# Kernel tuning notes

Measured on AMD Instinct MI355X. Metric: run time of the kernel, lower is better.

## Reference

```python
import jax, jax.numpy as jnp
import numpy as np

B, S, D = 4, 2048, 1024
E, H, K = 32, 128, 2


def setup_inputs() -> dict:
    key = jax.random.key(0)
    k1, k2, k3, k4 = jax.random.split(key, 4)
    scale_d = 1.0 / np.sqrt(D)
    scale_h = 1.0 / np.sqrt(H)
    return {
        "x": jax.random.normal(k1, (B, S, D), dtype=jnp.float32),
        "w_sel": jax.random.normal(k2, (E, D), dtype=jnp.float32) * scale_d,      # router Linear weight [E, D]
        "w_keys": jax.random.normal(k3, (E, D, H), dtype=jnp.float32) * scale_d,  # per-expert up-proj
        "w_values": jax.random.normal(k4, (E, H, D), dtype=jnp.float32) * scale_h, # per-expert down-proj
        "k": K,
    }


def reference(x, w_sel, w_keys, w_values, k):
    # Router: sigmoid gating + top-k expert selection per token.
    sel = jax.nn.sigmoid(jnp.einsum('bsd,ed->bse', x, w_sel))      # [B,S,E]
    sel_val, sel_idx = jax.lax.top_k(sel, k)                       # [B,S,k]
    n_exp = w_sel.shape[0]
    # Dense gate matrix: gate[b,s,e] = sum of sel_val over heads routed to e
    # (top_k indices are distinct, so this matches the per-head accumulation).
    gate = jnp.sum(jax.nn.one_hot(sel_idx, n_exp, dtype=x.dtype) * sel_val[..., None], axis=-2)  # [B,S,E]
    # Expert up-projection + ReLU for all experts (dense equivalent of the
    # per-token gathered keys[expert_idx](token); unselected experts are
    # zeroed by the gate so the math is identical).
    scores = jax.nn.relu(jnp.einsum('bsd,edh->bseh', x, w_keys))   # [B,S,E,H]
    weighted = scores * gate[..., None]                            # [B,S,E,H]
    out = jnp.einsum('bseh,ehd->bsd', weighted, w_values)          # [B,S,D]
    return out
```

## Files before the change

kernel.cpp:

```cpp
#include <hip/hip_runtime.h>
#include <cstdint>
#include <cstddef>

#define NTOK 8192
#define DIM  1024
#define NEXP 32
#define NH   128
#define TT   32
#define NSLOT 32
#define BK   128
#define RT   32
#define LCAP 1024

typedef __attribute__((ext_vector_type(8))) short short8;
typedef __attribute__((ext_vector_type(4))) float float4_;

static __device__ __forceinline__ unsigned short f2bf(float f) {
  unsigned u = __float_as_uint(f);
  return (unsigned short)((u + 0x7fffu + ((u >> 16) & 1u)) >> 16);
}
static __device__ __forceinline__ float bf2f(unsigned short h) {
  return __uint_as_float(((unsigned)h) << 16);
}
static __device__ __forceinline__ void gload_lds16(const unsigned short* g,
                                                   unsigned short* l) {
  __builtin_amdgcn_global_load_lds(
      (const __attribute__((address_space(1))) unsigned int*)(const void*)g,
      (__attribute__((address_space(3))) unsigned int*)(void*)l, 16, 0, 0);
}

__global__ __launch_bounds__(256) void prep_router_kernel(
    const float* __restrict__ x, const float* __restrict__ w_sel,
    const float* __restrict__ w_keys, const float* __restrict__ w_values,
    unsigned short* __restrict__ xbf, unsigned short* __restrict__ wk_t,
    unsigned short* __restrict__ wv_t,
    int* __restrict__ counts, unsigned* __restrict__ list)
{
  const int bid = blockIdx.x;
  const int tid = threadIdx.x;

  if (bid >= 256) {
    __shared__ float tile[32][33];
    const int lb = bid - 256;
    const float* src; unsigned short* dst; int R, C, e, t;
    if (lb < 4096) { src = w_keys;   dst = wk_t; R = DIM; C = NH;  e = lb >> 7;          t = lb & 127; }
    else           { src = w_values; dst = wv_t; R = NH;  C = DIM; e = (lb - 4096) >> 7; t = (lb - 4096) & 127; }
    const int tpc = C >> 5;
    const int r0 = (t / tpc) * 32;
    const int c0 = (t % tpc) * 32;
    const float* s = src + (size_t)e * R * C;
    unsigned short* d = dst + (size_t)e * R * C;

    const int i = tid >> 3;
    const int j = (tid & 7) * 4;
    float4 v = *(const float4*)(s + (size_t)(r0 + i) * C + c0 + j);
    tile[i][j] = v.x; tile[i][j + 1] = v.y; tile[i][j + 2] = v.z; tile[i][j + 3] = v.w;
    __syncthreads();
    unsigned lo = (unsigned)f2bf(tile[j + 0][i]) | ((unsigned)f2bf(tile[j + 1][i]) << 16);
    unsigned hi = (unsigned)f2bf(tile[j + 2][i]) | ((unsigned)f2bf(tile[j + 3][i]) << 16);
    uint2 u; u.x = lo; u.y = hi;
    *(uint2*)(d + (size_t)(c0 + i) * R + r0 + j) = u;
    return;
  }

  __shared__ __align__(16) float xs_t[64][36];
  __shared__ float ws[NEXP][65];
  __shared__ float S[RT][33];

  const int tok0 = bid * RT;
  const int tr   = tid >> 3;
  const int d8   = (tid & 7) * 8;
  const int tg4  = (tid & 7) * 4;

  float acc[4] = {0.f, 0.f, 0.f, 0.f};

  for (int dc = 0; dc < DIM; dc += 64) {
    const float* xp = x + (size_t)(tok0 + tr) * DIM + dc + d8;
    float4 a0 = *(const float4*)(xp);
    float4 a1 = *(const float4*)(xp + 4);
    xs_t[d8 + 0][tr] = a0.x; xs_t[d8 + 1][tr] = a0.y;
    xs_t[d8 + 2][tr] = a0.z; xs_t[d8 + 3][tr] = a0.w;
    xs_t[d8 + 4][tr] = a1.x; xs_t[d8 + 5][tr] = a1.y;
    xs_t[d8 + 6][tr] = a1.z; xs_t[d8 + 7][tr] = a1.w;
    uint4 u;
    u.x = (unsigned)f2bf(a0.x) | ((unsigned)f2bf(a0.y) << 16);
    u.y = (unsigned)f2bf(a0.z) | ((unsigned)f2bf(a0.w) << 16);
    u.z = (unsigned)f2bf(a1.x) | ((unsigned)f2bf(a1.y) << 16);
    u.w = (unsigned)f2bf(a1.z) | ((unsigned)f2bf(a1.w) << 16);
    *(uint4*)(xbf + (size_t)(tok0 + tr) * DIM + dc + d8) = u;

    const float* wp = w_sel + (size_t)tr * DIM + dc + d8;
    float4 b0 = *(const float4*)(wp);
    float4 b1 = *(const float4*)(wp + 4);
    ws[tr][d8 + 0] = b0.x; ws[tr][d8 + 1] = b0.y;
    ws[tr][d8 + 2] = b0.z; ws[tr][d8 + 3] = b0.w;
    ws[tr][d8 + 4] = b1.x; ws[tr][d8 + 5] = b1.y;
    ws[tr][d8 + 6] = b1.z; ws[tr][d8 + 7] = b1.w;
    __syncthreads();

    #pragma unroll 8
    for (int dd = 0; dd < 64; ++dd) {
      float w = ws[tr][dd];
      float4 xv = *(const float4*)&xs_t[dd][tg4];
      acc[0] += xv.x * w; acc[1] += xv.y * w;
      acc[2] += xv.z * w; acc[3] += xv.w * w;
    }
    __syncthreads();
  }

  #pragma unroll
  for (int j = 0; j < 4; ++j)
    S[tg4 + j][tr] = acc[j];
  __syncthreads();

  if (tid < RT) {
    const int t = tid;
    float m1 = -1e30f, m2 = -1e30f;
    int i1 = 0, i2 = 0;
    for (int ee = 0; ee < NEXP; ++ee) {
      float v = S[t][ee];
      if (v > m1)      { m2 = m1; i2 = i1; m1 = v; i1 = ee; }
      else if (v > m2) { m2 = v; i2 = ee; }
    }
    const int token = tok0 + t;
    float g1 = 1.f / (1.f + __expf(-m1));
    float g2 = 1.f / (1.f + __expf(-m2));
    unsigned e1 = ((unsigned)f2bf(g1) << 16) | ((unsigned)token << 1);
    unsigned e2 = ((unsigned)f2bf(g2) << 16) | ((unsigned)token << 1) | 1u;
    int p1 = atomicAdd(&counts[i1], 1);
    if (p1 < LCAP) list[i1 * LCAP + p1] = e1;
    int p2 = atomicAdd(&counts[i2], 1);
    if (p2 < LCAP) list[i2 * LCAP + p2] = e2;
  }
}

__global__ __launch_bounds__(256, 4) void ffn_kernel(
    const unsigned short* __restrict__ xbf,
    const unsigned short* __restrict__ wk_t,
    const unsigned short* __restrict__ wv_t,
    float* __restrict__ out,
    unsigned short* __restrict__ cont,
    const int* __restrict__ counts, const unsigned* __restrict__ list,
    int use_cont)
{
  const int bid = blockIdx.x;
  const int e   = bid & 31;
  const int cnt = min(counts[e], LCAP);
  const int t0  = (bid >> 5) * TT;
  if (t0 >= cnt) return;

  __shared__ __align__(16) unsigned short uni[8448];
  __shared__ unsigned short ss[TT][NH + 8];
  __shared__ int   toks[TT];
  __shared__ float gates[TT];
  unsigned short (*xsf)[4096] = (unsigned short (*)[4096])uni;
  unsigned short (*st)[264]   = (unsigned short (*)[264])uni;

  const int tid  = threadIdx.x;
  const int wave = tid >> 6;
  const int lane = tid & 63;
  const int quad = lane >> 4;
  const int l16  = lane & 15;

  const unsigned short* wkb = wk_t + (size_t)e * NH * DIM;
  const unsigned short* wvb = wv_t + (size_t)e * DIM * NH;
  const int n_tok = min(TT, cnt - t0);

  if (tid < TT) {
    int valid = tid < n_tok;
    unsigned en = valid ? list[e * LCAP + t0 + tid] : 0u;
    toks[tid]  = valid ? (int)(en & 0xffffu) : -1;
    gates[tid] = valid ? bf2f((unsigned short)(en >> 16)) : 0.f;
  }
  __syncthreads();

  const int smt  = wave >> 1;
  const int skk0 = (wave & 1) * 2;
  {
    int sl   = toks[smt * 16 + l16];
    int gtok = (sl < 0) ? 0 : (sl >> 1);
    const unsigned short* gsrc = xbf + (size_t)gtok * DIM + quad * 8;

    #pragma unroll
    for (int i2 = 0; i2 < 2; ++i2)
      gload_lds16(gsrc + (skk0 + i2) * 32, &xsf[0][(smt * 4 + skk0 + i2) * 512]);
    __syncthreads();

    float4_ acc[2][2];
    #pragma unroll
    for (int mt = 0; mt < 2; ++mt)
      #pragma unroll
      for (int nt = 0; nt < 2; ++nt) acc[mt][nt] = (float4_){0.f, 0.f, 0.f, 0.f};

    for (int ci = 0; ci < 8; ++ci) {
      const int dc = ci * BK;
      if (ci < 7) {
        const int nb = (ci + 1) & 1;
        #pragma unroll
        for (int i2 = 0; i2 < 2; ++i2)
          gload_lds16(gsrc + dc + BK + (skk0 + i2) * 32,
                      &xsf[nb][(smt * 4 + skk0 + i2) * 512]);
      }
      short8 b[4][2];
      #pragma unroll
      for (int kk = 0; kk < 4; ++kk)
        #pragma unroll
        for (int nt = 0; nt < 2; ++nt)
          b[kk][nt] = *(const short8*)(wkb +
              (size_t)(wave * 32 + nt * 16 + l16) * DIM + dc + kk * 32 + quad * 8);

      const unsigned short* xb = &xsf[ci & 1][0];
      #pragma unroll
      for (int kk = 0; kk < 4; ++kk) {
        #pragma unroll
        for (int mt = 0; mt < 2; ++mt) {
          short8 a = *(const short8*)(xb + (mt * 4 + kk) * 512 + lane * 8);
          #pragma unroll
          for (int nt = 0; nt < 2; ++nt)
            acc[mt][nt] = __builtin_amdgcn_mfma_f32_16x16x32_bf16(a, b[kk][nt], acc[mt][nt], 0, 0, 0);
        }
      }
      __syncthreads();
    }

    #pragma unroll
    for (int mt = 0; mt < 2; ++mt)
      #pragma unroll
      for (int nt = 0; nt < 2; ++nt)
        #pragma unroll
        for (int r = 0; r < 4; ++r) {
          int row = mt * 16 + quad * 4 + r;
          float v = fmaxf(acc[mt][nt][r], 0.f) * gates[row];
          ss[row][wave * 32 + nt * 16 + l16] = f2bf(v);
        }
  }
  __syncthreads();

  #pragma unroll 1
  for (int nc = 0; nc < 4; ++nc) {
    const int colbase = wave * 256 + nc * 64;
    float4_ o[2][4];
    #pragma unroll
    for (int mt = 0; mt < 2; ++mt)
      #pragma unroll
      for (int nt = 0; nt < 4; ++nt) o[mt][nt] = (float4_){0.f, 0.f, 0.f, 0.f};

    #pragma unroll
    for (int kk = 0; kk < 4; ++kk) {
      short8 bk[4];
      #pragma unroll
      for (int nt = 0; nt < 4; ++nt)
        bk[nt] = *(const short8*)(wvb +
            (size_t)(colbase + nt * 16 + l16) * NH + kk * 32 + quad * 8);
      short8 a0 = *(const short8*)&ss[l16][kk * 32 + quad * 8];
      short8 a1 = *(const short8*)&ss[16 + l16][kk * 32 + quad * 8];
      #pragma unroll
      for (int nt = 0; nt < 4; ++nt) {
        o[0][nt] = __builtin_amdgcn_mfma_f32_16x16x32_bf16(a0, bk[nt], o[0][nt], 0, 0, 0);
        o[1][nt] = __builtin_amdgcn_mfma_f32_16x16x32_bf16(a1, bk[nt], o[1][nt], 0, 0, 0);
      }
    }

    if (use_cont) {
      #pragma unroll
      for (int mt = 0; mt < 2; ++mt)
        #pragma unroll
        for (int nt = 0; nt < 4; ++nt)
          #pragma unroll
          for (int r = 0; r < 4; ++r)
            st[mt * 16 + quad * 4 + r][wave * 64 + nt * 16 + l16] = f2bf(o[mt][nt][r]);
      __syncthreads();
      #pragma unroll
      for (int q = 0; q < 4; ++q) {
        int idx = q * 256 + tid;
        int row = idx >> 5, seg = idx & 31;
        if (row < n_tok) {
          int sl2 = toks[row];
          size_t base = ((size_t)((sl2 & 1) * NTOK + (sl2 >> 1))) * DIM
                        + (seg >> 3) * 256 + nc * 64 + (seg & 7) * 8;
          *(short8*)&cont[base] = *(const short8*)&st[row][seg * 8];
        }
      }
      __syncthreads();
    } else {
      #pragma unroll
      for (int mt = 0; mt < 2; ++mt)
        #pragma unroll
        for (int r = 0; r < 4; ++r) {
          int row = mt * 16 + quad * 4 + r;
          if (row < n_tok) {
            size_t base = (size_t)(toks[row] >> 1) * DIM + colbase;
            #pragma unroll
            for (int nt = 0; nt < 4; ++nt)
              unsafeAtomicAdd(&out[base + nt * 16 + l16], o[mt][nt][r]);
          }
        }
    }
  }
}

__global__ __launch_bounds__(256) void combine_kernel(
    const unsigned short* __restrict__ cont, float* __restrict__ out)
{
  size_t i = ((size_t)blockIdx.x * 256 + threadIdx.x) * 8;
  uint4 a = *(const uint4*)(cont + i);
  uint4 b = *(const uint4*)(cont + (size_t)NTOK * DIM + i);
  float4 r0, r1;
  r0.x = bf2f((unsigned short)(a.x & 0xffff)) + bf2f((unsigned short)(b.x & 0xffff));
  r0.y = bf2f((unsigned short)(a.x >> 16))    + bf2f((unsigned short)(b.x >> 16));
  r0.z = bf2f((unsigned short)(a.y & 0xffff)) + bf2f((unsigned short)(b.y & 0xffff));
  r0.w = bf2f((unsigned short)(a.y >> 16))    + bf2f((unsigned short)(b.y >> 16));
  r1.x = bf2f((unsigned short)(a.z & 0xffff)) + bf2f((unsigned short)(b.z & 0xffff));
  r1.y = bf2f((unsigned short)(a.z >> 16))    + bf2f((unsigned short)(b.z >> 16));
  r1.z = bf2f((unsigned short)(a.w & 0xffff)) + bf2f((unsigned short)(b.w & 0xffff));
  r1.w = bf2f((unsigned short)(a.w >> 16))    + bf2f((unsigned short)(b.w >> 16));
  *(float4*)(out + i) = r0;
  *(float4*)(out + i + 4) = r1;
}

extern "C" void kernel_launch(void* const* d_in, const int* in_sizes, int n_in,
                              void* d_out, int out_size, void* d_ws, size_t ws_size,
                              hipStream_t stream) {
  (void)in_sizes; (void)n_in;
  const float* x        = (const float*)d_in[0];
  const float* w_sel    = (const float*)d_in[1];
  const float* w_keys   = (const float*)d_in[2];
  const float* w_values = (const float*)d_in[3];
  float* out = (float*)d_out;

  char* ws = (char*)d_ws;
  size_t off = 0;
  int*            counts = (int*)(ws + off);            off += 4096;
  unsigned*       list   = (unsigned*)(ws + off);       off += (size_t)NEXP * LCAP * 4;
  unsigned short* wk_t   = (unsigned short*)(ws + off); off += (size_t)NEXP * NH * DIM * 2;
  unsigned short* wv_t   = (unsigned short*)(ws + off); off += (size_t)NEXP * NH * DIM * 2;
  unsigned short* xbf    = (unsigned short*)(ws + off); off += (size_t)NTOK * DIM * 2;
  unsigned short* cont   = (unsigned short*)(ws + off);
  size_t need_full = off + (size_t)2 * NTOK * DIM * 2;
  const int use_cont = (ws_size >= need_full) ? 1 : 0;

  hipMemsetAsync(counts, 0, NEXP * sizeof(int), stream);

  prep_router_kernel<<<256 + 8192, 256, 0, stream>>>(x, w_sel, w_keys, w_values,
                                                     xbf, wk_t, wv_t, counts, list);

  if (!use_cont)
    hipMemsetAsync(out, 0, (size_t)out_size * sizeof(float), stream);

  ffn_kernel<<<NEXP * NSLOT, 256, 0, stream>>>(xbf, wk_t, wv_t, out, cont,
                                               counts, list, use_cont);

  if (use_cont)
    combine_kernel<<<NTOK * DIM / (256 * 8), 256, 0, stream>>>(cont, out);
}
```

Baseline: 225.6 us.

## Restructure router to per-wave D-split with scalar weight loads and larger transpose tiles

The router section now handles 64 tokens per block. Each of the four waves covers a quarter of D and keeps all 32 expert accumulators per token in registers. It reads w_sel through wave-uniform (scalar) loads and double-buffers the x staging in LDS, prefetching the next chunk, then sums the per-wave partials in shared memory before top-2. The weight transpose/convert blocks move from 32x32 to 64x64 tiles with wider 16-byte stores, cutting the block count from 8192 to 2048. The aim is to remove the router's LDS-bound inner loop and per-block overhead, at the cost of higher register pressure from the 32 accumulators and 16 cached x values.

```diff
diff --git a/kernel.cpp b/kernel.cpp
--- a/kernel.cpp
+++ b/kernel.cpp
@@ -9,8 +9,9 @@
 #define TT   32
 #define NSLOT 32
 #define BK   128
-#define RT   32
 #define LCAP 1024
+#define RTOK 64
+#define NRB  (NTOK / RTOK)
 
 typedef __attribute__((ext_vector_type(8))) short short8;
 typedef __attribute__((ext_vector_type(4))) float float4_;
@@ -36,89 +37,127 @@
     unsigned short* __restrict__ wv_t,
     int* __restrict__ counts, unsigned* __restrict__ list)
 {
+  __shared__ __align__(16) char smem[33792];
   const int bid = blockIdx.x;
   const int tid = threadIdx.x;
 
-  if (bid >= 256) {
-    __shared__ float tile[32][33];
-    const int lb = bid - 256;
-    const float* src; unsigned short* dst; int R, C, e, t;
-    if (lb < 4096) { src = w_keys;   dst = wk_t; R = DIM; C = NH;  e = lb >> 7;          t = lb & 127; }
-    else           { src = w_values; dst = wv_t; R = NH;  C = DIM; e = (lb - 4096) >> 7; t = (lb - 4096) & 127; }
-    const int tpc = C >> 5;
-    const int r0 = (t / tpc) * 32;
-    const int c0 = (t % tpc) * 32;
+  if (bid >= NRB) {
+    float (*tile)[65] = (float (*)[65])smem;
+    const int lb = bid - NRB;
+    const float* src; unsigned short* dst; int R, C, e, t, tpc;
+    if (lb < 1024) { src = w_keys;   dst = wk_t; R = DIM; C = NH;  e = lb >> 5;          t = lb & 31; tpc = 2; }
+    else           { src = w_values; dst = wv_t; R = NH;  C = DIM; e = (lb - 1024) >> 5; t = (lb - 1024) & 31; tpc = 16; }
+    const int r0 = (t / tpc) * 64;
+    const int c0 = (t % tpc) * 64;
     const float* s = src + (size_t)e * R * C;
     unsigned short* d = dst + (size_t)e * R * C;
 
-    const int i = tid >> 3;
-    const int j = (tid & 7) * 4;
-    float4 v = *(const float4*)(s + (size_t)(r0 + i) * C + c0 + j);
-    tile[i][j] = v.x; tile[i][j + 1] = v.y; tile[i][j + 2] = v.z; tile[i][j + 3] = v.w;
+    const int i  = tid >> 2;
+    const int j0 = (tid & 3) * 16;
+    #pragma unroll
+    for (int k4 = 0; k4 < 4; ++k4) {
+      float4 v = *(const float4*)(s + (size_t)(r0 + i) * C + c0 + j0 + k4 * 4);
+      tile[i][j0 + k4 * 4 + 0] = v.x;
+      tile[i][j0 + k4 * 4 + 1] = v.y;
+      tile[i][j0 + k4 * 4 + 2] = v.z;
+      tile[i][j0 + k4 * 4 + 3] = v.w;
+    }
     __syncthreads();
-    unsigned lo = (unsigned)f2bf(tile[j + 0][i]) | ((unsigned)f2bf(tile[j + 1][i]) << 16);
-    unsigned hi = (unsigned)f2bf(tile[j + 2][i]) | ((unsigned)f2bf(tile[j + 3][i]) << 16);
-    uint2 u; u.x = lo; u.y = hi;
-    *(uint2*)(d + (size_t)(c0 + i) * R + r0 + j) = u;
+    unsigned pk[8];
+    #pragma unroll
+    for (int k = 0; k < 8; ++k) {
+      unsigned lo = f2bf(tile[j0 + 2 * k][i]);
+      unsigned hi = f2bf(tile[j0 + 2 * k + 1][i]);
+      pk[k] = lo | (hi << 16);
+    }
+    uint4 u0; u0.x = pk[0]; u0.y = pk[1]; u0.z = pk[2]; u0.w = pk[3];
+    uint4 u1; u1.x = pk[4]; u1.y = pk[5]; u1.z = pk[6]; u1.w = pk[7];
+    unsigned short* dp = d + (size_t)(c0 + i) * R + r0 + j0;
+    *(uint4*)(dp)     = u0;
+    *(uint4*)(dp + 8) = u1;
     return;
   }
 
-  __shared__ __align__(16) float xs_t[64][36];
-  __shared__ float ws[NEXP][65];
-  __shared__ float S[RT][33];
-
-  const int tok0 = bid * RT;
-  const int tr   = tid >> 3;
-  const int d8   = (tid & 7) * 8;
-  const int tg4  = (tid & 7) * 4;
-
-  float acc[4] = {0.f, 0.f, 0.f, 0.f};
-
-  for (int dc = 0; dc < DIM; dc += 64) {
-    const float* xp = x + (size_t)(tok0 + tr) * DIM + dc + d8;
-    float4 a0 = *(const float4*)(xp);
-    float4 a1 = *(const float4*)(xp + 4);
-    xs_t[d8 + 0][tr] = a0.x; xs_t[d8 + 1][tr] = a0.y;
-    xs_t[d8 + 2][tr] = a0.z; xs_t[d8 + 3][tr] = a0.w;
-    xs_t[d8 + 4][tr] = a1.x; xs_t[d8 + 5][tr] = a1.y;
-    xs_t[d8 + 6][tr] = a1.z; xs_t[d8 + 7][tr] = a1.w;
-    uint4 u;
-    u.x = (unsigned)f2bf(a0.x) | ((unsigned)f2bf(a0.y) << 16);
-    u.y = (unsigned)f2bf(a0.z) | ((unsigned)f2bf(a0.w) << 16);
-    u.z = (unsigned)f2bf(a1.x) | ((unsigned)f2bf(a1.y) << 16);
-    u.w = (unsigned)f2bf(a1.z) | ((unsigned)f2bf(a1.w) << 16);
-    *(uint4*)(xbf + (size_t)(tok0 + tr) * DIM + dc + d8) = u;
-
-    const float* wp = w_sel + (size_t)tr * DIM + dc + d8;
-    float4 b0 = *(const float4*)(wp);
-    float4 b1 = *(const float4*)(wp + 4);
-    ws[tr][d8 + 0] = b0.x; ws[tr][d8 + 1] = b0.y;
-    ws[tr][d8 + 2] = b0.z; ws[tr][d8 + 3] = b0.w;
-    ws[tr][d8 + 4] = b1.x; ws[tr][d8 + 5] = b1.y;
-    ws[tr][d8 + 6] = b1.z; ws[tr][d8 + 7] = b1.w;
-    __syncthreads();
-
-    #pragma unroll 8
-    for (int dd = 0; dd < 64; ++dd) {
-      float w = ws[tr][dd];
-      float4 xv = *(const float4*)&xs_t[dd][tg4];
-      acc[0] += xv.x * w; acc[1] += xv.y * w;
-      acc[2] += xv.z * w; acc[3] += xv.w * w;
-    }
-    __syncthreads();
-  }
-
+  float (*stg)[2][16][65] = (float (*)[2][16][65])smem;
+  float (*sred)[64][33]   = (float (*)[64][33])smem;
+
+  const int wv   = tid >> 6;
+  const int ln   = tid & 63;
+  const int tok0 = bid * RTOK;
+  const int dw   = wv * 256;
+
+  const int st_t = ln >> 2;
+  const int st_f = (ln & 3) * 4;
+
+  float acc[NEXP];
   #pragma unroll
-  for (int j = 0; j < 4; ++j)
-    S[tg4 + j][tr] = acc[j];
+  for (int e = 0; e < NEXP; ++e) acc[e] = 0.f;
+
+  #pragma unroll
+  for (int p = 0; p < 4; ++p) {
+    const int t = st_t + p * 16;
+    const size_t gx = (size_t)(tok0 + t) * DIM + dw + st_f;
+    float4 v = *(const float4*)(x + gx);
+    stg[wv][0][st_f + 0][t] = v.x;
+    stg[wv][0][st_f + 1][t] = v.y;
+    stg[wv][0][st_f + 2][t] = v.z;
+    stg[wv][0][st_f + 3][t] = v.w;
+    uint2 u;
+    u.x = (unsigned)f2bf(v.x) | ((unsigned)f2bf(v.y) << 16);
+    u.y = (unsigned)f2bf(v.z) | ((unsigned)f2bf(v.w) << 16);
+    *(uint2*)(xbf + gx) = u;
+  }
+
+  for (int c = 0; c < 16; ++c) {
+    float4 nv[4];
+    if (c < 15) {
+      #pragma unroll
+      for (int p = 0; p < 4; ++p) {
+        const int t = st_t + p * 16;
+        nv[p] = *(const float4*)(x + (size_t)(tok0 + t) * DIM + dw + (c + 1) * 16 + st_f);
+      }
+    }
+
+    float xr[16];
+    #pragma unroll
+    for (int dd = 0; dd < 16; ++dd) xr[dd] = stg[wv][c & 1][dd][ln];
+
+    const float* wr = w_sel + __builtin_amdgcn_readfirstlane(dw + c * 16);
+    #pragma unroll
+    for (int e = 0; e < NEXP; ++e) {
+      #pragma unroll
+      for (int dd = 0; dd < 16; ++dd)
+        acc[e] = fmaf(xr[dd], wr[e * DIM + dd], acc[e]);
+    }
+
+    if (c < 15) {
+      const int nb = (c + 1) & 1;
+      #pragma unroll
+      for (int p = 0; p < 4; ++p) {
+        const int t = st_t + p * 16;
+        stg[wv][nb][st_f + 0][t] = nv[p].x;
+        stg[wv][nb][st_f + 1][t] = nv[p].y;
+        stg[wv][nb][st_f + 2][t] = nv[p].z;
+        stg[wv][nb][st_f + 3][t] = nv[p].w;
+        uint2 u;
+        u.x = (unsigned)f2bf(nv[p].x) | ((unsigned)f2bf(nv[p].y) << 16);
+        u.y = (unsigned)f2bf(nv[p].z) | ((unsigned)f2bf(nv[p].w) << 16);
+        *(uint2*)(xbf + (size_t)(tok0 + t) * DIM + dw + (c + 1) * 16 + st_f) = u;
+      }
+    }
+  }
+
   __syncthreads();
-
-  if (tid < RT) {
+  #pragma unroll
+  for (int e = 0; e < NEXP; ++e) sred[wv][ln][e] = acc[e];
+  __syncthreads();
+
+  if (tid < RTOK) {
     const int t = tid;
     float m1 = -1e30f, m2 = -1e30f;
     int i1 = 0, i2 = 0;
     for (int ee = 0; ee < NEXP; ++ee) {
-      float v = S[t][ee];
+      float v = sred[0][t][ee] + sred[1][t][ee] + sred[2][t][ee] + sred[3][t][ee];
       if (v > m1)      { m2 = m1; i2 = i1; m1 = v; i1 = ee; }
       else if (v > m2) { m2 = v; i2 = ee; }
     }
@@ -341,7 +380,7 @@
 
   hipMemsetAsync(counts, 0, NEXP * sizeof(int), stream);
 
-  prep_router_kernel<<<256 + 8192, 256, 0, stream>>>(x, w_sel, w_keys, w_values,
+  prep_router_kernel<<<NRB + 2048, 256, 0, stream>>>(x, w_sel, w_keys, w_values,
                                                      xbf, wk_t, wv_t, counts, list);
 
   if (!use_cont)
```

Result: slower. 414.5 us (+83.7%).

## Restructure prep kernel: direct-global router, larger transpose tiles, separate bf16 convert blocks

Applied to the files above, without the earlier changes.

The router blocks now compute logits straight from global memory, with each thread producing four expert dot products for one token, so the LDS staging and per-chunk barriers are gone. The weight transpose moves from 32x32 to 64x64 tiles with 16-byte stores, cutting the block count from 8192 to 2048. The x-to-bf16 conversion is split out into its own 512 blocks instead of riding on the router blocks. This spreads the prep work more evenly across the GPU, at the cost of reading x twice (once for routing, once for conversion) and relying on the cache for w_sel reuse.

```diff
diff --git a/kernel.cpp b/kernel.cpp
--- a/kernel.cpp
+++ b/kernel.cpp
@@ -11,6 +11,9 @@
 #define BK   128
 #define RT   32
 #define LCAP 1024
+#define NRB  (NTOK / RT)
+#define NTRB 2048
+#define NCVB 512
 
 typedef __attribute__((ext_vector_type(8))) short short8;
 typedef __attribute__((ext_vector_type(4))) float float4_;
@@ -36,101 +39,138 @@
     unsigned short* __restrict__ wv_t,
     int* __restrict__ counts, unsigned* __restrict__ list)
 {
+  __shared__ __align__(16) char smem[16640];
   const int bid = blockIdx.x;
   const int tid = threadIdx.x;
 
-  if (bid >= 256) {
-    __shared__ float tile[32][33];
-    const int lb = bid - 256;
-    const float* src; unsigned short* dst; int R, C, e, t;
-    if (lb < 4096) { src = w_keys;   dst = wk_t; R = DIM; C = NH;  e = lb >> 7;          t = lb & 127; }
-    else           { src = w_values; dst = wv_t; R = NH;  C = DIM; e = (lb - 4096) >> 7; t = (lb - 4096) & 127; }
-    const int tpc = C >> 5;
-    const int r0 = (t / tpc) * 32;
-    const int c0 = (t % tpc) * 32;
+  if (bid < NRB) {
+    float (*S)[33] = (float (*)[33])smem;
+    const int tok0 = bid * RT;
+    const int t  = tid >> 3;
+    const int eg = tid & 7;
+    const float* xp = x + (size_t)(tok0 + t) * DIM;
+    const float* wp = w_sel + (size_t)(eg * 4) * DIM;
+
+    float acc0 = 0.f, acc1 = 0.f, acc2 = 0.f, acc3 = 0.f;
+    for (int d = 0; d < DIM; d += 8) {
+      float4 xa = *(const float4*)(xp + d);
+      float4 xb = *(const float4*)(xp + d + 4);
+      const float* w0 = wp + d;
+      float4 wa0 = *(const float4*)(w0);
+      float4 wb0 = *(const float4*)(w0 + 4);
+      float4 wa1 = *(const float4*)(w0 + DIM);
+      float4 wb1 = *(const float4*)(w0 + DIM + 4);
+      float4 wa2 = *(const float4*)(w0 + 2 * DIM);
+      float4 wb2 = *(const float4*)(w0 + 2 * DIM + 4);
+      float4 wa3 = *(const float4*)(w0 + 3 * DIM);
+      float4 wb3 = *(const float4*)(w0 + 3 * DIM + 4);
+      acc0 = fmaf(xa.x, wa0.x, acc0); acc0 = fmaf(xa.y, wa0.y, acc0);
+      acc0 = fmaf(xa.z, wa0.z, acc0); acc0 = fmaf(xa.w, wa0.w, acc0);
+      acc0 = fmaf(xb.x, wb0.x, acc0); acc0 = fmaf(xb.y, wb0.y, acc0);
+      acc0 = fmaf(xb.z, wb0.z, acc0); acc0 = fmaf(xb.w, wb0.w, acc0);
+      acc1 = fmaf(xa.x, wa1.x, acc1); acc1 = fmaf(xa.y, wa1.y, acc1);
+      acc1 = fmaf(xa.z, wa1.z, acc1); acc1 = fmaf(xa.w, wa1.w, acc1);
+      acc1 = fmaf(xb.x, wb1.x, acc1); acc1 = fmaf(xb.y, wb1.y, acc1);
+      acc1 = fmaf(xb.z, wb1.z, acc1); acc1 = fmaf(xb.w, wb1.w, acc1);
+      acc2 = fmaf(xa.x, wa2.x, acc2); acc2 = fmaf(xa.y, wa2.y, acc2);
+      acc2 = fmaf(xa.z, wa2.z, acc2); acc2 = fmaf(xa.w, wa2.w, acc2);
+      acc2 = fmaf(xb.x, wb2.x, acc2); acc2 = fmaf(xb.y, wb2.y, acc2);
+      acc2 = fmaf(xb.z, wb2.z, acc2); acc2 = fmaf(xb.w, wb2.w, acc2);
+      acc3 = fmaf(xa.x, wa3.x, acc3); acc3 = fmaf(xa.y, wa3.y, acc3);
+      acc3 = fmaf(xa.z, wa3.z, acc3); acc3 = fmaf(xa.w, wa3.w, acc3);
+      acc3 = fmaf(xb.x, wb3.x, acc3); acc3 = fmaf(xb.y, wb3.y, acc3);
+      acc3 = fmaf(xb.z, wb3.z, acc3); acc3 = fmaf(xb.w, wb3.w, acc3);
+    }
+    S[t][eg * 4 + 0] = acc0;
+    S[t][eg * 4 + 1] = acc1;
+    S[t][eg * 4 + 2] = acc2;
+    S[t][eg * 4 + 3] = acc3;
+    __syncthreads();
+
+    if (tid < RT) {
+      const int tt = tid;
+      float m1 = -1e30f, m2 = -1e30f;
+      int i1 = 0, i2 = 0;
+      for (int ee = 0; ee < NEXP; ++ee) {
+        float v = S[tt][ee];
+        if (v > m1)      { m2 = m1; i2 = i1; m1 = v; i1 = ee; }
+        else if (v > m2) { m2 = v; i2 = ee; }
+      }
+      const int token = tok0 + tt;
+      float g1 = 1.f / (1.f + __expf(-m1));
+      float g2 = 1.f / (1.f + __expf(-m2));
+      unsigned e1 = ((unsigned)f2bf(g1) << 16) | ((unsigned)token << 1);
+      unsigned e2 = ((unsigned)f2bf(g2) << 16) | ((unsigned)token << 1) | 1u;
+      int p1 = atomicAdd(&counts[i1], 1);
+      if (p1 < LCAP) list[i1 * LCAP + p1] = e1;
+      int p2 = atomicAdd(&counts[i2], 1);
+      if (p2 < LCAP) list[i2 * LCAP + p2] = e2;
+    }
+    return;
+  }
+
+  if (bid < NRB + NTRB) {
+    float (*tile)[65] = (float (*)[65])smem;
+    const int lb = bid - NRB;
+    const float* src; unsigned short* dst; int R, C, e, t, tpc;
+    if (lb < 1024) { src = w_keys;   dst = wk_t; R = DIM; C = NH;  e = lb >> 5;          t = lb & 31; tpc = 2; }
+    else           { src = w_values; dst = wv_t; R = NH;  C = DIM; e = (lb - 1024) >> 5; t = (lb - 1024) & 31; tpc = 16; }
+    const int r0 = (t / tpc) * 64;
+    const int c0 = (t % tpc) * 64;
     const float* s = src + (size_t)e * R * C;
     unsigned short* d = dst + (size_t)e * R * C;
 
-    const int i = tid >> 3;
-    const int j = (tid & 7) * 4;
-    float4 v = *(const float4*)(s + (size_t)(r0 + i) * C + c0 + j);
-    tile[i][j] = v.x; tile[i][j + 1] = v.y; tile[i][j + 2] = v.z; tile[i][j + 3] = v.w;
+    const int rr = tid >> 4;
+    const int cc = (tid & 15) * 4;
+    #pragma unroll
+    for (int k4 = 0; k4 < 4; ++k4) {
+      float4 v = *(const float4*)(s + (size_t)(r0 + rr + k4 * 16) * C + c0 + cc);
+      tile[rr + k4 * 16][cc + 0] = v.x;
+      tile[rr + k4 * 16][cc + 1] = v.y;
+      tile[rr + k4 * 16][cc + 2] = v.z;
+      tile[rr + k4 * 16][cc + 3] = v.w;
+    }
     __syncthreads();
-    unsigned lo = (unsigned)f2bf(tile[j + 0][i]) | ((unsigned)f2bf(tile[j + 1][i]) << 16);
-    unsigned hi = (unsigned)f2bf(tile[j + 2][i]) | ((unsigned)f2bf(tile[j + 3][i]) << 16);
-    uint2 u; u.x = lo; u.y = hi;
-    *(uint2*)(d + (size_t)(c0 + i) * R + r0 + j) = u;
+
+    const int jj = (tid & 7) * 8;
+    const int oo = tid >> 3;
+    #pragma unroll
+    for (int p = 0; p < 2; ++p) {
+      const int o = p * 32 + oo;
+      unsigned pk[4];
+      #pragma unroll
+      for (int k = 0; k < 4; ++k) {
+        unsigned lo = f2bf(tile[jj + 2 * k][o]);
+        unsigned hi = f2bf(tile[jj + 2 * k + 1][o]);
+        pk[k] = lo | (hi << 16);
+      }
+      uint4 u; u.x = pk[0]; u.y = pk[1]; u.z = pk[2]; u.w = pk[3];
+      *(uint4*)(d + (size_t)(c0 + o) * R + r0 + jj) = u;
+    }
     return;
   }
 
-  __shared__ __align__(16) float xs_t[64][36];
-  __shared__ float ws[NEXP][65];
-  __shared__ float S[RT][33];
-
-  const int tok0 = bid * RT;
-  const int tr   = tid >> 3;
-  const int d8   = (tid & 7) * 8;
-  const int tg4  = (tid & 7) * 4;
-
-  float acc[4] = {0.f, 0.f, 0.f, 0.f};
-
-  for (int dc = 0; dc < DIM; dc += 64) {
-    const float* xp = x + (size_t)(tok0 + tr) * DIM + dc + d8;
-    float4 a0 = *(const float4*)(xp);
-    float4 a1 = *(const float4*)(xp + 4);
-    xs_t[d8 + 0][tr] = a0.x; xs_t[d8 + 1][tr] = a0.y;
-    xs_t[d8 + 2][tr] = a0.z; xs_t[d8 + 3][tr] = a0.w;
-    xs_t[d8 + 4][tr] = a1.x; xs_t[d8 + 5][tr] = a1.y;
-    xs_t[d8 + 6][tr] = a1.z; xs_t[d8 + 7][tr] = a1.w;
-    uint4 u;
-    u.x = (unsigned)f2bf(a0.x) | ((unsigned)f2bf(a0.y) << 16);
-    u.y = (unsigned)f2bf(a0.z) | ((unsigned)f2bf(a0.w) << 16);
-    u.z = (unsigned)f2bf(a1.x) | ((unsigned)f2bf(a1.y) << 16);
-    u.w = (unsigned)f2bf(a1.z) | ((unsigned)f2bf(a1.w) << 16);
-    *(uint4*)(xbf + (size_t)(tok0 + tr) * DIM + dc + d8) = u;
-
-    const float* wp = w_sel + (size_t)tr * DIM + dc + d8;
-    float4 b0 = *(const float4*)(wp);
-    float4 b1 = *(const float4*)(wp + 4);
-    ws[tr][d8 + 0] = b0.x; ws[tr][d8 + 1] = b0.y;
-    ws[tr][d8 + 2] = b0.z; ws[tr][d8 + 3] = b0.w;
-    ws[tr][d8 + 4] = b1.x; ws[tr][d8 + 5] = b1.y;
-    ws[tr][d8 + 6] = b1.z; ws[tr][d8 + 7] = b1.w;
-    __syncthreads();
-
-    #pragma unroll 8
-    for (int dd = 0; dd < 64; ++dd) {
-      float w = ws[tr][dd];
-      float4 xv = *(const float4*)&xs_t[dd][tg4];
-      acc[0] += xv.x * w; acc[1] += xv.y * w;
-      acc[2] += xv.z * w; acc[3] += xv.w * w;
-    }
-    __syncthreads();
-  }
-
-  #pragma unroll
-  for (int j = 0; j < 4; ++j)
-    S[tg4 + j][tr] = acc[j];
-  __syncthreads();
-
-  if (tid < RT) {
-    const int t = tid;
-    float m1 = -1e30f, m2 = -1e30f;
-    int i1 = 0, i2 = 0;
-    for (int ee = 0; ee < NEXP; ++ee) {
-      float v = S[t][ee];
-      if (v > m1)      { m2 = m1; i2 = i1; m1 = v; i1 = ee; }
-      else if (v > m2) { m2 = v; i2 = ee; }
-    }
-    const int token = tok0 + t;
-    float g1 = 1.f / (1.f + __expf(-m1));
-    float g2 = 1.f / (1.f + __expf(-m2));
-    unsigned e1 = ((unsigned)f2bf(g1) << 16) | ((unsigned)token << 1);
-    unsigned e2 = ((unsigned)f2bf(g2) << 16) | ((unsigned)token << 1) | 1u;
-    int p1 = atomicAdd(&counts[i1], 1);
-    if (p1 < LCAP) list[i1 * LCAP + p1] = e1;
-    int p2 = atomicAdd(&counts[i2], 1);
-    if (p2 < LCAP) list[i2 * LCAP + p2] = e2;
+  {
+    const int lb = bid - NRB - NTRB;
+    #pragma unroll
+    for (int q = 0; q < 4; ++q) {
+      const size_t off = (size_t)lb * 16384 + (size_t)q * 4096 + (size_t)tid * 16;
+      float4 v0 = *(const float4*)(x + off);
+      float4 v1 = *(const float4*)(x + off + 4);
+      float4 v2 = *(const float4*)(x + off + 8);
+      float4 v3 = *(const float4*)(x + off + 12);
+      uint4 u0, u1;
+      u0.x = (unsigned)f2bf(v0.x) | ((unsigned)f2bf(v0.y) << 16);
+      u0.y = (unsigned)f2bf(v0.z) | ((unsigned)f2bf(v0.w) << 16);
+      u0.z = (unsigned)f2bf(v1.x) | ((unsigned)f2bf(v1.y) << 16);
+      u0.w = (unsigned)f2bf(v1.z) | ((unsigned)f2bf(v1.w) << 16);
+      u1.x = (unsigned)f2bf(v2.x) | ((unsigned)f2bf(v2.y) << 16);
+      u1.y = (unsigned)f2bf(v2.z) | ((unsigned)f2bf(v2.w) << 16);
+      u1.z = (unsigned)f2bf(v3.x) | ((unsigned)f2bf(v3.y) << 16);
+      u1.w = (unsigned)f2bf(v3.z) | ((unsigned)f2bf(v3.w) << 16);
+      *(uint4*)(xbf + off)     = u0;
+      *(uint4*)(xbf + off + 8) = u1;
+    }
   }
 }
 
@@ -341,8 +381,8 @@
 
   hipMemsetAsync(counts, 0, NEXP * sizeof(int), stream);
 
-  prep_router_kernel<<<256 + 8192, 256, 0, stream>>>(x, w_sel, w_keys, w_values,
-                                                     xbf, wk_t, wv_t, counts, list);
+  prep_router_kernel<<<NRB + NTRB + NCVB, 256, 0, stream>>>(
+      x, w_sel, w_keys, w_values, xbf, wk_t, wv_t, counts, list);
 
   if (!use_cont)
     hipMemsetAsync(out, 0, (size_t)out_size * sizeof(float), stream);
```

Result: slower. 313.9 us (+39.1%).
